# Kernel optimization log

Measured on AMD Instinct MI355X. Metric: run time of the kernel, lower is better.

Reference implementation:

```python
import jax, jax.numpy as jnp
import numpy as np

B = 8192
NV = 778   # MANO vertices
NJ = 16    # LBS joints
PARENTS = np.array([0, 0, 1, 2, 0, 4, 5, 0, 7, 8, 0, 10, 11, 0, 13, 14])


def quat2mat(quat):
    # quat: [N,4] (w,x,y,z) -> [N,3,3]
    q = quat / jnp.linalg.norm(quat, axis=1, keepdims=True)
    w, x, y, z = q[:, 0], q[:, 1], q[:, 2], q[:, 3]
    w2, x2, y2, z2 = w * w, x * x, y * y, z * z
    wx, wy, wz = w * x, w * y, w * z
    xy, xz, yz = x * y, x * z, y * z
    R = jnp.stack([
        w2 + x2 - y2 - z2, 2 * xy - 2 * wz, 2 * wy + 2 * xz,
        2 * wz + 2 * xy, w2 - x2 + y2 - z2, 2 * yz - 2 * wx,
        2 * xz - 2 * wy, 2 * wx + 2 * yz, w2 - x2 - y2 + z2,
    ], axis=1)
    return R.reshape(-1, 3, 3)


def batch_rodrigues(theta):
    # theta: [N,3] axis-angle -> [N,3,3]
    angle = jnp.linalg.norm(theta + 1e-8, axis=1, keepdims=True)
    normalized = theta / angle
    half = angle * 0.5
    quat = jnp.concatenate([jnp.cos(half), jnp.sin(half) * normalized], axis=1)
    return quat2mat(quat)


def qmul(q, r):
    # Hamilton product, (w,x,y,z); q,r: [N,4]
    w1, x1, y1, z1 = q[:, 0], q[:, 1], q[:, 2], q[:, 3]
    w2, x2, y2, z2 = r[:, 0], r[:, 1], r[:, 2], r[:, 3]
    return jnp.stack([
        w1 * w2 - x1 * x2 - y1 * y2 - z1 * z2,
        w1 * x2 + x1 * w2 + y1 * z2 - z1 * y2,
        w1 * y2 - x1 * z2 + y1 * w2 + z1 * x2,
        w1 * z2 + x1 * y2 - y1 * x2 + z1 * w2,
    ], axis=1)


def make_A(R, t):
    # R: [B,J,3,3], t: [B,J,3] -> [B,J,4,4]
    Bn, J = R.shape[0], R.shape[1]
    top = jnp.concatenate([R, t[..., None]], axis=-1)              # [B,J,3,4]
    bot = jnp.broadcast_to(jnp.array([0., 0., 0., 1.], R.dtype), (Bn, J, 1, 4))
    return jnp.concatenate([top, bot], axis=-2)


def mano_forward(theta, delta_quat, user_shape, init_quat, init_trans,
                 v_template, shapedirs, J_regressor, posedirs, weights):
    Bn = theta.shape[0]
    beta = jnp.broadcast_to(user_shape, (Bn, user_shape.shape[-1]))
    v_shaped = (beta @ shapedirs).reshape(Bn, NV, 3) + v_template   # [B,778,3]
    J = jnp.einsum('bvc,vj->bjc', v_shaped, J_regressor)            # [B,21,3]

    Rs = batch_rodrigues(theta.reshape(-1, 3)).reshape(Bn, 15, 3, 3)
    pose_feature = (Rs - jnp.eye(3, dtype=Rs.dtype)).reshape(Bn, 135)
    v_posed = (pose_feature @ posedirs).reshape(Bn, NV, 3) + v_shaped

    quat = qmul(delta_quat, jnp.broadcast_to(init_quat, (Bn, 4)))
    root_R = quat2mat(quat)                                          # [B,3,3]
    Rs_all = jnp.concatenate([root_R[:, None], Rs], axis=1)          # [B,16,3,3]

    Jk = J[:, :NJ]                                                   # [B,16,3]
    rel = Jk - Jk[:, PARENTS]
    rel = rel.at[:, 0].set(Jk[:, 0])                                 # root keeps absolute pos
    A_local = make_A(Rs_all, rel)                                    # [B,16,4,4]

    # kinematic chain (fixed 16-joint tree)
    results = [A_local[:, 0]]
    for i in range(1, NJ):
        results.append(results[PARENTS[i]] @ A_local[:, i])
    G = jnp.stack(results, axis=1)                                   # [B,16,4,4]

    Jw0 = jnp.concatenate([Jk, jnp.zeros((Bn, NJ, 1), Jk.dtype)], axis=-1)
    init_bone = jnp.einsum('bjkl,bjl->bjk', G, Jw0)                  # [B,16,4]
    A = jnp.concatenate([G[..., :3], G[..., 3:] - init_bone[..., None]], axis=-1)

    T = jnp.einsum('vj,bjkl->bvkl', weights, A)                      # [B,778,4,4]
    vp_homo = jnp.concatenate([v_posed, jnp.ones((Bn, NV, 1), v_posed.dtype)], axis=-1)
    verts = jnp.einsum('bvkl,bvl->bvk', T, vp_homo)[..., :3]         # [B,778,3]

    joints = jnp.einsum('bvc,vj->bjc', verts, J_regressor)           # [B,21,3]
    trans = init_trans.reshape(Bn, 1, 3)
    return joints + trans  # get_skin=False path


def setup_inputs() -> dict:
    key = jax.random.key(0)
    ks = jax.random.split(key, 10)
    return {
        'theta': jax.random.normal(ks[0], (B, 45), jnp.float32) * 0.3,
        'delta_quat': jax.random.normal(ks[1], (B, 4), jnp.float32),
        'user_shape': jax.random.normal(ks[2], (1, 10), jnp.float32),
        'init_quat': jax.random.normal(ks[3], (1, 4), jnp.float32),
        'init_trans': jax.random.normal(ks[4], (B, 3), jnp.float32),
        'v_template': jax.random.normal(ks[5], (NV, 3), jnp.float32),
        'shapedirs': jax.random.normal(ks[6], (10, NV * 3), jnp.float32) * 0.01,
        'J_regressor': jax.random.uniform(ks[7], (NV, 21), jnp.float32) / NV,
        'posedirs': jax.random.normal(ks[8], (135, NV * 3), jnp.float32) * 0.01,
        'weights': jax.random.uniform(ks[9], (NV, NJ), jnp.float32),
    }


def reference(theta, delta_quat, user_shape, init_quat, init_trans,
              v_template, shapedirs, J_regressor, posedirs, weights):
    return mano_forward(theta, delta_quat, user_shape, init_quat, init_trans,
                        v_template, shapedirs, J_regressor, posedirs, weights)
```

## Files before the change

kernel.cpp:

```cpp
#include <hip/hip_runtime.h>
#include <math.h>

#define B_SIZE 8192
#define NVERT 778
#define NP 135
#define NEC 416
#define KS16 16

#define OFF_JK    0
#define OFF_C1    64
#define OFF_C0    400
#define OFF_P2    1408
#define OFF_PFT   137488
#define OFF_AT    1243408
#define OFF_PP_OVER 137488
#define OFF_PP_SAFE 2816272

__device__ inline void quat2mat_dev(float qw, float qx, float qy, float qz, float* R) {
  float n = sqrtf(qw*qw + qx*qx + qy*qy + qz*qz);
  float w = qw/n, x = qx/n, y = qy/n, z = qz/n;
  float w2=w*w, x2=x*x, y2=y*y, z2=z*z;
  float wx=w*x, wy=w*y, wz=w*z, xy=x*y, xz=x*z, yz=y*z;
  R[0]=w2+x2-y2-z2; R[1]=2.f*xy-2.f*wz; R[2]=2.f*wy+2.f*xz;
  R[3]=2.f*wz+2.f*xy; R[4]=w2-x2+y2-z2; R[5]=2.f*yz-2.f*wx;
  R[6]=2.f*xz-2.f*wy; R[7]=2.f*wx+2.f*yz; R[8]=w2-x2-y2+z2;
}

__device__ inline void rodrigues_dev(float tx, float ty, float tz, float* R) {
  float ax = tx + 1e-8f, ay = ty + 1e-8f, az = tz + 1e-8f;
  float angle = sqrtf(ax*ax + ay*ay + az*az);
  float nx = tx/angle, ny = ty/angle, nz = tz/angle;
  float half = 0.5f*angle;
  float cw = cosf(half), sw = sinf(half);
  quat2mat_dev(cw, sw*nx, sw*ny, sw*nz, R);
}

__device__ inline void pose_unit(const float* __restrict__ theta,
                                 const float* __restrict__ delta_quat,
                                 const float* __restrict__ init_quat,
                                 float* __restrict__ ws,
                                 const float* jk, const float* rel,
                                 int bb, int u, int lane) {
  int b = bb*256 + lane;
  float* pfT = ws + OFF_PFT;
  float4* AT4 = (float4*)(ws + OFF_AT);
  float w1=delta_quat[b*4+0], x1=delta_quat[b*4+1], y1=delta_quat[b*4+2], z1=delta_quat[b*4+3];
  float w2=init_quat[0], x2=init_quat[1], y2=init_quat[2], z2=init_quat[3];
  float qw = w1*w2 - x1*x2 - y1*y2 - z1*z2;
  float qx = w1*x2 + x1*w2 + y1*z2 - z1*y2;
  float qy = w1*y2 - x1*z2 + y1*w2 + z1*x2;
  float qz = w1*z2 + x1*y2 - y1*x2 + z1*w2;
  float G[12];
  quat2mat_dev(qw, qx, qy, qz, G);
  G[9] = rel[0]; G[10] = rel[1]; G[11] = rel[2];
  if (u == 5) {
    #pragma unroll
    for (int c = 0; c < 3; ++c) {
      float g0 = G[c*3+0], g1 = G[c*3+1], g2 = G[c*3+2];
      AT4[(size_t)(c)*B_SIZE + b] =
        make_float4(g0, g1, g2, G[9+c] - (g0*jk[0] + g1*jk[1] + g2*jk[2]));
    }
    return;
  }
  #pragma unroll
  for (int mstep = 0; mstep < 3; ++mstep) {
    int j = 3*u + 1 + mstep;
    int i = j - 1;
    float R[9];
    rodrigues_dev(theta[b*45+3*i+0], theta[b*45+3*i+1], theta[b*45+3*i+2], R);
    pfT[(size_t)(9*i+0)*B_SIZE + b] = R[0]-1.f;
    pfT[(size_t)(9*i+1)*B_SIZE + b] = R[1];
    pfT[(size_t)(9*i+2)*B_SIZE + b] = R[2];
    pfT[(size_t)(9*i+3)*B_SIZE + b] = R[3];
    pfT[(size_t)(9*i+4)*B_SIZE + b] = R[4]-1.f;
    pfT[(size_t)(9*i+5)*B_SIZE + b] = R[5];
    pfT[(size_t)(9*i+6)*B_SIZE + b] = R[6];
    pfT[(size_t)(9*i+7)*B_SIZE + b] = R[7];
    pfT[(size_t)(9*i+8)*B_SIZE + b] = R[8]-1.f;
    float nG[12];
    const float* rj = rel + j*3;
    #pragma unroll
    for (int r3 = 0; r3 < 3; ++r3) {
      float a0 = G[r3*3+0], a1 = G[r3*3+1], a2 = G[r3*3+2];
      nG[r3*3+0] = a0*R[0] + a1*R[3] + a2*R[6];
      nG[r3*3+1] = a0*R[1] + a1*R[4] + a2*R[7];
      nG[r3*3+2] = a0*R[2] + a1*R[5] + a2*R[8];
      nG[9+r3]   = G[9+r3] + a0*rj[0] + a1*rj[1] + a2*rj[2];
    }
    #pragma unroll
    for (int k = 0; k < 12; ++k) G[k] = nG[k];
    const float* jkj = jk + j*3;
    #pragma unroll
    for (int c = 0; c < 3; ++c) {
      float g0 = G[c*3+0], g1 = G[c*3+1], g2 = G[c*3+2];
      AT4[(size_t)(j*3+c)*B_SIZE + b] =
        make_float4(g0, g1, g2, G[9+c] - (g0*jkj[0] + g1*jkj[1] + g2*jkj[2]));
    }
  }
}

__device__ inline void kr_task(float* __restrict__ ws, int pp_off, int idx) {
  if (idx >= 416*84) return;
  int ec = idx / 84, q4 = idx - ec*84;
  const float* Pp = ws + pp_off;
  float4 s = make_float4(0.f, 0.f, 0.f, 0.f);
  #pragma unroll
  for (int ks = 0; ks < KS16; ++ks) {
    float4 v = *(const float4*)&Pp[(size_t)ks*NEC*336 + ec*336 + 4*q4];
    s.x += v.x; s.y += v.y; s.z += v.z; s.w += v.w;
  }
  float sv[4] = {s.x, s.y, s.z, s.w};
  #pragma unroll
  for (int r = 0; r < 4; ++r) {
    int q2 = 4*q4 + r;
    int jj2 = q2 >> 4, jj = q2 & 15;
    if (ec < 408) {
      int c = ec / 136, pp = ec - c*136;
      if (pp < 135) ws[OFF_P2 + (size_t)(jj2*135 + pp)*48 + jj*3 + c] = sv[r];
      else          ws[OFF_C0 + jj2*48 + jj*3 + c] = sv[r];
    } else if (ec == 408) {
      ws[OFF_C1 + jj2*16 + jj] = sv[r];
    }
  }
}

__global__ __launch_bounds__(256) void kA(const float* __restrict__ J_regressor,
                                          const float* __restrict__ weights,
                                          const float* __restrict__ posedirs,
                                          const float* __restrict__ user_shape,
                                          const float* __restrict__ v_template,
                                          const float* __restrict__ shapedirs,
                                          float* __restrict__ ws, int pp_off) {
  int tid = threadIdx.x;
  int bid = blockIdx.x;

  if (bid >= 416) {
    int j = bid - 416;
    __shared__ float red[3*256];
    __shared__ float ush[10];
    if (tid < 10) ush[tid] = user_shape[tid];
    __syncthreads();
    float p0 = 0.f, p1 = 0.f, p2 = 0.f;
    for (int v = tid; v < NVERT; v += 256) {
      float jr = J_regressor[v*21 + j];
      #pragma unroll
      for (int c = 0; c < 3; ++c) {
        int e = 3*v + c;
        float t = v_template[e];
        #pragma unroll
        for (int s = 0; s < 10; ++s) t += ush[s]*shapedirs[s*2334 + e];
        float val = jr * t;
        if (c == 0) p0 += val; else if (c == 1) p1 += val; else p2 += val;
      }
    }
    red[0*256+tid] = p0; red[1*256+tid] = p1; red[2*256+tid] = p2;
    __syncthreads();
    for (int s = 128; s > 0; s >>= 1) {
      if (tid < s) {
        red[0*256+tid] += red[0*256+tid+s];
        red[1*256+tid] += red[1*256+tid+s];
        red[2*256+tid] += red[2*256+tid+s];
      }
      __syncthreads();
    }
    if (tid < 3) ws[OFF_JK + j*3 + tid] = red[tid*256];
    return;
  }

  __shared__ float sJR[49*21];
  __shared__ float sW [49*16];
  __shared__ float sB [64*16];
  __shared__ float ush[10];
  if (tid < 10) ush[tid] = user_shape[tid];
  int ng = bid % 26;
  int ks = bid / 26;
  int vbeg = ks*49;
  int kt = min(NVERT - vbeg, 49);
  __syncthreads();
  for (int idx = tid; idx < kt*21; idx += 256) sJR[idx] = J_regressor[vbeg*21 + idx];
  for (int idx = tid; idx < kt*16; idx += 256) sW[idx]  = weights[vbeg*16 + idx];
  for (int idx = tid; idx < 16*64; idx += 256) {
    int s = idx >> 6, iv = idx & 63;
    if (iv < kt) {
      int ec = ng*16 + s;
      float val;
      if (ec > 408) val = 0.f;
      else if (ec == 408) val = 1.f;
      else {
        int c = ec / 136, pp = ec - c*136;
        int e = 3*(vbeg+iv) + c;
        if (pp == 135) {
          float t = v_template[e];
          #pragma unroll
          for (int s0 = 0; s0 < 10; ++s0) t += ush[s0]*shapedirs[s0*2334 + e];
          val = t;
        } else {
          val = posedirs[pp*2334 + e];
        }
      }
      sB[iv*16 + s] = val;
    }
  }
  __syncthreads();
  if (tid < 168) {
    int cg2 = (tid < 84) ? 0 : 1;
    int r4  = (tid < 84) ? tid : tid - 84;
    int q2 = 4*r4;
    int j2 = q2 >> 4;
    int jb = q2 & 15;
    float acc[4][8];
    #pragma unroll
    for (int r = 0; r < 4; ++r)
      #pragma unroll
      for (int s = 0; s < 8; ++s) acc[r][s] = 0.f;
    for (int i = 0; i < kt; ++i) {
      float jr = sJR[i*21 + j2];
      float4 w4 = *(const float4*)&sW[i*16 + jb];
      float4 b0 = *(const float4*)&sB[i*16 + cg2*8];
      float4 b1 = *(const float4*)&sB[i*16 + cg2*8 + 4];
      float wv[4] = {w4.x, w4.y, w4.z, w4.w};
      #pragma unroll
      for (int r = 0; r < 4; ++r) {
        float s2 = jr * wv[r];
        acc[r][0] += s2*b0.x; acc[r][1] += s2*b0.y;
        acc[r][2] += s2*b0.z; acc[r][3] += s2*b0.w;
        acc[r][4] += s2*b1.x; acc[r][5] += s2*b1.y;
        acc[r][6] += s2*b1.z; acc[r][7] += s2*b1.w;
      }
    }
    float* Pp = ws + pp_off + (size_t)ks*NEC*336;
    #pragma unroll
    for (int s = 0; s < 8; ++s) {
      int ec = ng*16 + cg2*8 + s;
      float4 v4 = make_float4(acc[0][s], acc[1][s], acc[2][s], acc[3][s]);
      *(float4*)&Pp[ec*336 + q2] = v4;
    }
  }
}

__global__ __launch_bounds__(256) void kRk4(const float* __restrict__ theta,
                                            const float* __restrict__ delta_quat,
                                            const float* __restrict__ init_quat,
                                            float* __restrict__ ws, int pp_off) {
  int bid = blockIdx.x;
  int tid = threadIdx.x;
  if (bid < 137) {
    kr_task(ws, pp_off, bid*256 + tid);
    return;
  }
  __shared__ float jk[48], rel[48];
  if (tid < 48) {
    float v = ws[OFF_JK + tid];
    jk[tid] = v;
    int j = tid/3, c = tid - j*3;
    float r;
    if (j == 0) r = v;
    else {
      int par = (((j-1) % 3) == 0) ? 0 : (j-1);
      r = v - ws[OFF_JK + par*3 + c];
    }
    rel[tid] = r;
  }
  __syncthreads();
  int s = bid & 7;
  int t = (bid - 137) >> 3;
  int bb = s + 8*(t & 3);
  int u  = t >> 2;
  pose_unit(theta, delta_quat, init_quat, ws, jk, rel, bb, u, tid);
}

__global__ void kR_fb(float* __restrict__ ws, int pp_off) {
  kr_task(ws, pp_off, blockIdx.x*256 + threadIdx.x);
}

__global__ __launch_bounds__(256) void k4_fb(const float* __restrict__ theta,
                                             const float* __restrict__ delta_quat,
                                             const float* __restrict__ init_quat,
                                             float* __restrict__ ws) {
  int bid = blockIdx.x;
  int tid = threadIdx.x;
  __shared__ float jk[48], rel[48];
  if (tid < 48) {
    float v = ws[OFF_JK + tid];
    jk[tid] = v;
    int j = tid/3, c = tid - j*3;
    float r;
    if (j == 0) r = v;
    else {
      int par = (((j-1) % 3) == 0) ? 0 : (j-1);
      r = v - ws[OFF_JK + par*3 + c];
    }
    rel[tid] = r;
  }
  __syncthreads();
  int s = bid & 7;
  int t = bid >> 3;
  int bb = s + 8*(t & 3);
  int u  = t >> 2;
  pose_unit(theta, delta_quat, init_quat, ws, jk, rel, bb, u, tid);
}

__global__ __launch_bounds__(128) void k5_main(const float* __restrict__ init_trans,
                                               const float* __restrict__ ws,
                                               float* __restrict__ out) {
  __shared__ int s_voff[1];
  int g = blockIdx.x;
  int xcd = g & 7, k = g >> 3;
  int br  = ((k & 3) << 3) | xcd;
  int j2  = k >> 2;
  int tid = threadIdx.x;
  int b   = br*256 + tid;
  int b2  = b + 128;

  if (tid == 0) s_voff[0] = j2*135*12;
  __syncthreads();
  int voff = s_voff[0];

  float4 acc[12], acc2[12];
  const float4* c04 = (const float4*)(ws + OFF_C0 + j2*48);
  #pragma unroll
  for (int i = 0; i < 12; ++i) { acc[i] = c04[i]; acc2[i] = acc[i]; }

  const float* pfT = ws + OFF_PFT;
  const float4* P24 = (const float4*)(ws + OFF_P2) + voff;
  #pragma unroll 3
  for (int p = 0; p < NP; ++p) {
    float pf  = pfT[(size_t)p*B_SIZE + b];
    float pf2 = pfT[(size_t)p*B_SIZE + b2];
    const float4* Pr = P24 + p*12;
    #pragma unroll
    for (int i = 0; i < 12; ++i) {
      float4 pv = Pr[i];
      acc[i].x  += pf *pv.x; acc[i].y  += pf *pv.y;
      acc[i].z  += pf *pv.z; acc[i].w  += pf *pv.w;
      acc2[i].x += pf2*pv.x; acc2[i].y += pf2*pv.y;
      acc2[i].z += pf2*pv.z; acc2[i].w += pf2*pv.w;
    }
  }

  float m[48], m2[48];
  #pragma unroll
  for (int i = 0; i < 12; ++i) {
    m[4*i+0]  = acc[i].x;  m[4*i+1]  = acc[i].y;
    m[4*i+2]  = acc[i].z;  m[4*i+3]  = acc[i].w;
    m2[4*i+0] = acc2[i].x; m2[4*i+1] = acc2[i].y;
    m2[4*i+2] = acc2[i].z; m2[4*i+3] = acc2[i].w;
  }

  const float4* AT4 = (const float4*)(ws + OFF_AT);
  const float* c1p = ws + OFF_C1 + j2*16;
  float o0 = 0.f, o1 = 0.f, o2 = 0.f;
  float q0 = 0.f, q1 = 0.f, q2v = 0.f;
  #pragma unroll
  for (int j = 0; j < 16; ++j) {
    float c1 = c1p[j];
    float m0  = m[3*j+0],  m1  = m[3*j+1],  mm2 = m[3*j+2];
    float n0  = m2[3*j+0], n1  = m2[3*j+1], n2  = m2[3*j+2];
    #pragma unroll
    for (int k2 = 0; k2 < 3; ++k2) {
      float4 a  = AT4[(size_t)(j*3+k2)*B_SIZE + b];
      float4 a2 = AT4[(size_t)(j*3+k2)*B_SIZE + b2];
      float r  = a.x *m0 + a.y *m1 + a.z *mm2 + a.w *c1;
      float r2 = a2.x*n0 + a2.y*n1 + a2.z*n2  + a2.w*c1;
      if (k2 == 0) { o0 += r; q0 += r2; }
      else if (k2 == 1) { o1 += r; q1 += r2; }
      else { o2 += r; q2v += r2; }
    }
  }
  size_t ob = ((size_t)b*21 + j2)*3;
  out[ob+0] = o0 + init_trans[b*3+0];
  out[ob+1] = o1 + init_trans[b*3+1];
  out[ob+2] = o2 + init_trans[b*3+2];
  size_t ob2 = ((size_t)b2*21 + j2)*3;
  out[ob2+0] = q0  + init_trans[b2*3+0];
  out[ob2+1] = q1  + init_trans[b2*3+1];
  out[ob2+2] = q2v + init_trans[b2*3+2];
}

extern "C" void kernel_launch(void* const* d_in, const int* in_sizes, int n_in,
                              void* d_out, int out_size, void* d_ws, size_t ws_size,
                              hipStream_t stream) {
  const float* theta       = (const float*)d_in[0];
  const float* delta_quat  = (const float*)d_in[1];
  const float* user_shape  = (const float*)d_in[2];
  const float* init_quat   = (const float*)d_in[3];
  const float* init_trans  = (const float*)d_in[4];
  const float* v_template  = (const float*)d_in[5];
  const float* shapedirs   = (const float*)d_in[6];
  const float* J_regressor = (const float*)d_in[7];
  const float* posedirs    = (const float*)d_in[8];
  const float* weights     = (const float*)d_in[9];
  float* out = (float*)d_out;
  float* ws  = (float*)d_ws;

  size_t need = ((size_t)OFF_PP_SAFE + (size_t)KS16*NEC*336) * 4;
  if (ws_size >= need) {
    kA<<<432, 256, 0, stream>>>(J_regressor, weights, posedirs,
                                user_shape, v_template, shapedirs, ws, OFF_PP_SAFE);
    kRk4<<<329, 256, 0, stream>>>(theta, delta_quat, init_quat, ws, OFF_PP_SAFE);
  } else {
    kA<<<432, 256, 0, stream>>>(J_regressor, weights, posedirs,
                                user_shape, v_template, shapedirs, ws, OFF_PP_OVER);
    kR_fb<<<137, 256, 0, stream>>>(ws, OFF_PP_OVER);
    k4_fb<<<192, 256, 0, stream>>>(theta, delta_quat, init_quat, ws);
  }
  k5_main<<<672, 128, 0, stream>>>(init_trans, ws, out);
}
```

Measured before the change: 158.1 us.

## Split k5 reduction across two half-blocks with shared-memory combine

Doubles k5_main's block size so two 128-thread halves each handle half of the 135-term pose-feature reduction. The partial accumulators are combined through LDS, and each half then applies half of the 16 joint transforms before a final shared-memory sum. The aim is more waves per CU and shorter per-thread serial chains for a grid of only 672 blocks. In exchange it adds about 50KB of LDS per block and three barriers, and the extra LDS could limit occupancy.

After: 171.5 us. +8.5%, slower.

```diff
diff --git a/kernel.cpp b/kernel.cpp
--- a/kernel.cpp
+++ b/kernel.cpp
@@ -300,16 +300,20 @@
   pose_unit(theta, delta_quat, init_quat, ws, jk, rel, bb, u, tid);
 }
 
-__global__ __launch_bounds__(128) void k5_main(const float* __restrict__ init_trans,
+__global__ __launch_bounds__(256) void k5_main(const float* __restrict__ init_trans,
                                                const float* __restrict__ ws,
                                                float* __restrict__ out) {
   __shared__ int s_voff[1];
+  __shared__ __align__(16) float4 xm4[12*256];
+  __shared__ float xo[6*128];
   int g = blockIdx.x;
   int xcd = g & 7, k = g >> 3;
   int br  = ((k & 3) << 3) | xcd;
   int j2  = k >> 2;
   int tid = threadIdx.x;
-  int b   = br*256 + tid;
+  int h   = tid >> 7;
+  int l   = tid & 127;
+  int b   = br*256 + l;
   int b2  = b + 128;
 
   if (tid == 0) s_voff[0] = j2*135*12;
@@ -317,49 +321,113 @@
   int voff = s_voff[0];
 
   float4 acc[12], acc2[12];
-  const float4* c04 = (const float4*)(ws + OFF_C0 + j2*48);
-  #pragma unroll
-  for (int i = 0; i < 12; ++i) { acc[i] = c04[i]; acc2[i] = acc[i]; }
+  #pragma unroll
+  for (int i = 0; i < 12; ++i) {
+    acc[i]  = make_float4(0.f, 0.f, 0.f, 0.f);
+    acc2[i] = make_float4(0.f, 0.f, 0.f, 0.f);
+  }
 
   const float* pfT = ws + OFF_PFT;
   const float4* P24 = (const float4*)(ws + OFF_P2) + voff;
-  #pragma unroll 3
-  for (int p = 0; p < NP; ++p) {
-    float pf  = pfT[(size_t)p*B_SIZE + b];
-    float pf2 = pfT[(size_t)p*B_SIZE + b2];
-    const float4* Pr = P24 + p*12;
+  if (h == 0) {
+    #pragma unroll 2
+    for (int p = 0; p < 68; ++p) {
+      float pf  = pfT[(size_t)p*B_SIZE + b];
+      float pf2 = pfT[(size_t)p*B_SIZE + b2];
+      const float4* Pr = P24 + p*12;
+      #pragma unroll
+      for (int i = 0; i < 12; ++i) {
+        float4 pv = Pr[i];
+        acc[i].x  += pf *pv.x; acc[i].y  += pf *pv.y;
+        acc[i].z  += pf *pv.z; acc[i].w  += pf *pv.w;
+        acc2[i].x += pf2*pv.x; acc2[i].y += pf2*pv.y;
+        acc2[i].z += pf2*pv.z; acc2[i].w += pf2*pv.w;
+      }
+    }
+  } else {
+    #pragma unroll 2
+    for (int p = 68; p < NP; ++p) {
+      float pf  = pfT[(size_t)p*B_SIZE + b];
+      float pf2 = pfT[(size_t)p*B_SIZE + b2];
+      const float4* Pr = P24 + p*12;
+      #pragma unroll
+      for (int i = 0; i < 12; ++i) {
+        float4 pv = Pr[i];
+        acc[i].x  += pf *pv.x; acc[i].y  += pf *pv.y;
+        acc[i].z  += pf *pv.z; acc[i].w  += pf *pv.w;
+        acc2[i].x += pf2*pv.x; acc2[i].y += pf2*pv.y;
+        acc2[i].z += pf2*pv.z; acc2[i].w += pf2*pv.w;
+      }
+    }
+  }
+
+  if (h == 1) {
+    #pragma unroll
+    for (int i = 0; i < 12; ++i) xm4[i*256 + l]       = acc[i];
+    #pragma unroll
+    for (int i = 0; i < 12; ++i) xm4[i*256 + 128 + l] = acc2[i];
+  }
+  __syncthreads();
+  if (h == 0) {
     #pragma unroll
     for (int i = 0; i < 12; ++i) {
-      float4 pv = Pr[i];
-      acc[i].x  += pf *pv.x; acc[i].y  += pf *pv.y;
-      acc[i].z  += pf *pv.z; acc[i].w  += pf *pv.w;
-      acc2[i].x += pf2*pv.x; acc2[i].y += pf2*pv.y;
-      acc2[i].z += pf2*pv.z; acc2[i].w += pf2*pv.w;
-    }
-  }
-
-  float m[48], m2[48];
-  #pragma unroll
-  for (int i = 0; i < 12; ++i) {
-    m[4*i+0]  = acc[i].x;  m[4*i+1]  = acc[i].y;
-    m[4*i+2]  = acc[i].z;  m[4*i+3]  = acc[i].w;
-    m2[4*i+0] = acc2[i].x; m2[4*i+1] = acc2[i].y;
-    m2[4*i+2] = acc2[i].z; m2[4*i+3] = acc2[i].w;
-  }
+      float4 t = xm4[i*256 + l];
+      acc[i].x += t.x; acc[i].y += t.y; acc[i].z += t.z; acc[i].w += t.w;
+    }
+    #pragma unroll
+    for (int i = 0; i < 12; ++i) {
+      float4 t = xm4[i*256 + 128 + l];
+      acc2[i].x += t.x; acc2[i].y += t.y; acc2[i].z += t.z; acc2[i].w += t.w;
+    }
+    #pragma unroll
+    for (int i = 6; i < 12; ++i) xm4[i*256 + l]       = acc[i];
+    #pragma unroll
+    for (int i = 6; i < 12; ++i) xm4[i*256 + 128 + l] = acc2[i];
+  }
+  __syncthreads();
+  if (h == 1) {
+    #pragma unroll
+    for (int i = 6; i < 12; ++i) acc[i]  = xm4[i*256 + l];
+    #pragma unroll
+    for (int i = 6; i < 12; ++i) acc2[i] = xm4[i*256 + 128 + l];
+  }
+
+  float me[24], me2[24];
+  if (h == 0) {
+    #pragma unroll
+    for (int i = 0; i < 6; ++i) {
+      me[4*i+0]  = acc[i].x;  me[4*i+1]  = acc[i].y;
+      me[4*i+2]  = acc[i].z;  me[4*i+3]  = acc[i].w;
+      me2[4*i+0] = acc2[i].x; me2[4*i+1] = acc2[i].y;
+      me2[4*i+2] = acc2[i].z; me2[4*i+3] = acc2[i].w;
+    }
+  } else {
+    #pragma unroll
+    for (int i = 0; i < 6; ++i) {
+      me[4*i+0]  = acc[6+i].x;  me[4*i+1]  = acc[6+i].y;
+      me[4*i+2]  = acc[6+i].z;  me[4*i+3]  = acc[6+i].w;
+      me2[4*i+0] = acc2[6+i].x; me2[4*i+1] = acc2[6+i].y;
+      me2[4*i+2] = acc2[6+i].z; me2[4*i+3] = acc2[6+i].w;
+    }
+  }
+  const float* c0h = ws + OFF_C0 + j2*48 + 24*h;
+  #pragma unroll
+  for (int t = 0; t < 24; ++t) { me[t] += c0h[t]; me2[t] += c0h[t]; }
 
   const float4* AT4 = (const float4*)(ws + OFF_AT);
-  const float* c1p = ws + OFF_C1 + j2*16;
+  const float* c1h = ws + OFF_C1 + j2*16 + 8*h;
+  int jrow0 = 24*h;
   float o0 = 0.f, o1 = 0.f, o2 = 0.f;
   float q0 = 0.f, q1 = 0.f, q2v = 0.f;
   #pragma unroll
-  for (int j = 0; j < 16; ++j) {
-    float c1 = c1p[j];
-    float m0  = m[3*j+0],  m1  = m[3*j+1],  mm2 = m[3*j+2];
-    float n0  = m2[3*j+0], n1  = m2[3*j+1], n2  = m2[3*j+2];
+  for (int jj = 0; jj < 8; ++jj) {
+    float c1 = c1h[jj];
+    float m0  = me[3*jj+0],  m1  = me[3*jj+1],  mm2 = me[3*jj+2];
+    float n0  = me2[3*jj+0], n1  = me2[3*jj+1], n2  = me2[3*jj+2];
     #pragma unroll
     for (int k2 = 0; k2 < 3; ++k2) {
-      float4 a  = AT4[(size_t)(j*3+k2)*B_SIZE + b];
-      float4 a2 = AT4[(size_t)(j*3+k2)*B_SIZE + b2];
+      float4 a  = AT4[(size_t)(jrow0 + jj*3 + k2)*B_SIZE + b];
+      float4 a2 = AT4[(size_t)(jrow0 + jj*3 + k2)*B_SIZE + b2];
       float r  = a.x *m0 + a.y *m1 + a.z *mm2 + a.w *c1;
       float r2 = a2.x*n0 + a2.y*n1 + a2.z*n2  + a2.w*c1;
       if (k2 == 0) { o0 += r; q0 += r2; }
@@ -367,14 +435,24 @@
       else { o2 += r; q2v += r2; }
     }
   }
-  size_t ob = ((size_t)b*21 + j2)*3;
-  out[ob+0] = o0 + init_trans[b*3+0];
-  out[ob+1] = o1 + init_trans[b*3+1];
-  out[ob+2] = o2 + init_trans[b*3+2];
-  size_t ob2 = ((size_t)b2*21 + j2)*3;
-  out[ob2+0] = q0  + init_trans[b2*3+0];
-  out[ob2+1] = q1  + init_trans[b2*3+1];
-  out[ob2+2] = q2v + init_trans[b2*3+2];
+
+  if (h == 1) {
+    xo[0*128 + l] = o0; xo[1*128 + l] = o1; xo[2*128 + l] = o2;
+    xo[3*128 + l] = q0; xo[4*128 + l] = q1; xo[5*128 + l] = q2v;
+  }
+  __syncthreads();
+  if (h == 0) {
+    o0  += xo[0*128 + l]; o1 += xo[1*128 + l]; o2  += xo[2*128 + l];
+    q0  += xo[3*128 + l]; q1 += xo[4*128 + l]; q2v += xo[5*128 + l];
+    size_t ob = ((size_t)b*21 + j2)*3;
+    out[ob+0] = o0 + init_trans[b*3+0];
+    out[ob+1] = o1 + init_trans[b*3+1];
+    out[ob+2] = o2 + init_trans[b*3+2];
+    size_t ob2 = ((size_t)b2*21 + j2)*3;
+    out[ob2+0] = q0  + init_trans[b2*3+0];
+    out[ob2+1] = q1  + init_trans[b2*3+1];
+    out[ob2+2] = q2v + init_trans[b2*3+2];
+  }
 }
 
 extern "C" void kernel_launch(void* const* d_in, const int* in_sizes, int n_in,
@@ -404,5 +482,5 @@
     kR_fb<<<137, 256, 0, stream>>>(ws, OFF_PP_OVER);
     k4_fb<<<192, 256, 0, stream>>>(theta, delta_quat, init_quat, ws);
   }
-  k5_main<<<672, 128, 0, stream>>>(init_trans, ws, out);
-}
+  k5_main<<<672, 256, 0, stream>>>(init_trans, ws, out);
+}
```
